# Kernel optimization log

Measured on AMD Instinct MI355X. Metric: run time of the kernel, lower is better.

Reference implementation:

```python
import jax, jax.numpy as jnp
import numpy as np


def setup_inputs() -> dict:
    key = jax.random.key(0)
    ks = jax.random.split(key, 5)
    B, H, W, C = 64, 14, 14, 2048
    x = jax.random.normal(ks[0], (B, H, W, C), dtype=jnp.float32)
    # Glorot-ish scaled 1x1 conv weights (stored as [Cin, Cout])
    W1 = jax.random.normal(ks[1], (C, 64), dtype=jnp.float32) * (1.0 / np.sqrt(C))
    W2 = jax.random.normal(ks[2], (64, 16), dtype=jnp.float32) * (1.0 / np.sqrt(64))
    W3 = jax.random.normal(ks[3], (16, 8), dtype=jnp.float32) * (1.0 / np.sqrt(16))
    W4 = jax.random.normal(ks[4], (8, 1), dtype=jnp.float32) * (1.0 / np.sqrt(8))
    return {
        "x": x,
        "W1": W1, "b1": jnp.zeros((64,), jnp.float32),
        "W2": W2, "b2": jnp.zeros((16,), jnp.float32),
        "W3": W3, "b3": jnp.zeros((8,), jnp.float32),
        "W4": W4, "b4": jnp.zeros((1,), jnp.float32),
    }


def reference(x, W1, b1, W2, b2, W3, b3, W4, b4):
    # Dropout is identity at inference time.
    # 1x1 convs == per-pixel matmuls over channel dim.
    h = jax.nn.relu(jnp.einsum('bhwc,cd->bhwd', x, W1) + b1)   # [B,H,W,64]
    h = jax.nn.relu(jnp.einsum('bhwc,cd->bhwd', h, W2) + b2)   # [B,H,W,16]
    h = jax.nn.relu(jnp.einsum('bhwc,cd->bhwd', h, W3) + b3)   # [B,H,W,8]
    a = jax.nn.sigmoid(jnp.einsum('bhwc,cd->bhwd', h, W4) + b4)  # [B,H,W,1]
    # 'upsample' frozen ones-conv == broadcast of a over 2048 channels.
    gap_features = jnp.mean(a * x, axis=(1, 2))  # [B, 2048]
    gap_mask = jnp.mean(a, axis=(1, 2))          # [B, 1] (same value for all 2048 chans)
    return gap_features / gap_mask               # [B, 2048]
```

## Files before the change

### kernel.cpp

```cpp
#include <hip/hip_runtime.h>
#include <math.h>

#define NPIX 12544
#define CIN  2048
#define NB   64
#define PPIX 196
#define BPIMG 14
#define PXB  14
#define NBLK (NB * BPIMG)

typedef short  bf16x8 __attribute__((ext_vector_type(8)));
typedef short  bf16x4 __attribute__((ext_vector_type(4)));
typedef float  f32x4  __attribute__((ext_vector_type(4)));

__device__ inline unsigned short f2bf(float f) {
    unsigned int u = __float_as_uint(f);
    u = (u + 0x7fffu + ((u >> 16) & 1u)) >> 16;
    return (unsigned short)u;
}
__device__ inline float bf2f(unsigned short u) {
    return __uint_as_float((unsigned int)u << 16);
}

__global__ __launch_bounds__(256) void conv_w1(
    const float* __restrict__ W1, unsigned short* __restrict__ W1t)
{
    const int id = blockIdx.x * 256 + threadIdx.x;
    const int n = id >> 11;
    const int k = id & 2047;
    W1t[id] = f2bf(W1[k * 64 + n]);
}

__global__ __launch_bounds__(512, 4) void fused_attn_gap(
    const float* __restrict__ x, const unsigned short* __restrict__ W1t,
    const float* __restrict__ b1,
    const float* __restrict__ W2, const float* __restrict__ b2,
    const float* __restrict__ W3, const float* __restrict__ b3,
    const float* __restrict__ W4, const float* __restrict__ b4,
    float* __restrict__ part2, float* __restrict__ asum_part)
{
    __shared__ short xs[256 * 16 * 8];
    __shared__ float h1s[16][68];
    __shared__ float h2s[16][16];
    __shared__ float h3s[16][8];
    __shared__ float a_s[16];

    const int t    = threadIdx.x;
    const int wv   = t >> 6;
    const int lane = t & 63;
    const int l15  = lane & 15;
    const int q    = lane >> 4;
    const int blk  = blockIdx.x;
    const size_t pix0 = (size_t)blk * PXB;

    const int tp = t >> 5;
    const int tc = t & 31;
    float4 xv[16];
    if (tp < PXB) {
        const float* xp = x + (pix0 + tp) * (size_t)CIN + tc * 4;
#pragma unroll
        for (int i = 0; i < 16; ++i)
            xv[i] = *(const float4*)(xp + i * 128);
    } else {
#pragma unroll
        for (int i = 0; i < 16; ++i) xv[i] = make_float4(0.f, 0.f, 0.f, 0.f);
    }
    if (t < 256)
        *(f32x4*)&h1s[t >> 4][(t & 15) * 4] = *(const f32x4*)(b1 + (t & 15) * 4);
#pragma unroll
    for (int i = 0; i < 16; ++i) {
        const int k = tc * 4 + i * 128;
        const int g = k >> 3;
        const int e = k & 7;
        bf16x4 w;
        w[0] = (short)f2bf(xv[i].x); w[1] = (short)f2bf(xv[i].y);
        w[2] = (short)f2bf(xv[i].z); w[3] = (short)f2bf(xv[i].w);
        *(bf16x4*)&xs[(g * 16 + tp) * 8 + e] = w;
    }
    __syncthreads();

    const unsigned short* wr = W1t + (size_t)l15 * CIN + wv * 256 + q * 8;
    const bf16x8* xsv = (const bf16x8*)xs;
    const int gq = wv * 32 + q;

    f32x4 acc[4] = {{0,0,0,0},{0,0,0,0},{0,0,0,0},{0,0,0,0}};
    bf16x8 wA[4], wB[4];
#pragma unroll
    for (int ct = 0; ct < 4; ++ct)
        wA[ct] = *(const bf16x8*)(wr + (size_t)ct * 16 * CIN);
#pragma unroll
    for (int i = 0; i < 8; ++i) {
        if (i < 7) {
            if ((i & 1) == 0) {
#pragma unroll
                for (int ct = 0; ct < 4; ++ct)
                    wB[ct] = *(const bf16x8*)(wr + (size_t)ct * 16 * CIN + 32 * (i + 1));
            } else {
#pragma unroll
                for (int ct = 0; ct < 4; ++ct)
                    wA[ct] = *(const bf16x8*)(wr + (size_t)ct * 16 * CIN + 32 * (i + 1));
            }
        }
        const bf16x8 av = xsv[(gq + i * 4) * 16 + l15];
        if ((i & 1) == 0) {
#pragma unroll
            for (int ct = 0; ct < 4; ++ct)
                acc[ct] = __builtin_amdgcn_mfma_f32_16x16x32_bf16(av, wA[ct], acc[ct], 0, 0, 0);
        } else {
#pragma unroll
            for (int ct = 0; ct < 4; ++ct)
                acc[ct] = __builtin_amdgcn_mfma_f32_16x16x32_bf16(av, wB[ct], acc[ct], 0, 0, 0);
        }
    }
#pragma unroll
    for (int ct = 0; ct < 4; ++ct)
#pragma unroll
        for (int r = 0; r < 4; ++r)
            atomicAdd(&h1s[q * 4 + r][ct * 16 + l15], acc[ct][r]);
    __syncthreads();

    const int p = t >> 4;
    const int j = t & 15;
    if (t < 256) {
        float s = b2[j];
#pragma unroll
        for (int k = 0; k < 64; ++k)
            s = fmaf(fmaxf(h1s[p][k], 0.f), W2[k * 16 + j], s);
        h2s[p][j] = fmaxf(s, 0.f);
    }
    __syncthreads();
    if (t < 256 && j < 8) {
        float s = b3[j];
#pragma unroll
        for (int k = 0; k < 16; ++k) s = fmaf(h2s[p][k], W3[k * 8 + j], s);
        h3s[p][j] = fmaxf(s, 0.f);
    }
    __syncthreads();
    if (t < 256 && j == 0) {
        float z = b4[0];
#pragma unroll
        for (int k = 0; k < 8; ++k) z = fmaf(h3s[p][k], W4[k], z);
        a_s[p] = (p < PXB) ? (1.f / (1.f + expf(-z))) : 0.f;
    }
    __syncthreads();

    if (t == 0) {
        float s = 0.f;
#pragma unroll
        for (int pp = 0; pp < PXB; ++pp) s += a_s[pp];
        asum_part[blk] = s;
    }

    const float ap = a_s[l15];
#pragma unroll
    for (int gi = 0; gi < 8; ++gi) {
        const int g = wv * 32 + q * 8 + gi;
        const bf16x8 v = xsv[g * 16 + l15];
        float sarr[8];
#pragma unroll
        for (int e = 0; e < 8; ++e)
            sarr[e] = ap * bf2f((unsigned short)v[e]);
#pragma unroll
        for (int m = 1; m < 16; m <<= 1)
#pragma unroll
            for (int e = 0; e < 8; ++e)
                sarr[e] += __shfl_xor(sarr[e], m, 16);
        if (l15 == 0) {
            float* dst = part2 + (size_t)blk * CIN + g * 8;
            *(float4*)dst       = make_float4(sarr[0], sarr[1], sarr[2], sarr[3]);
            *(float4*)(dst + 4) = make_float4(sarr[4], sarr[5], sarr[6], sarr[7]);
        }
    }
}

__global__ __launch_bounds__(512) void gap_final(
    const float* __restrict__ asum_part, const float* __restrict__ part2,
    float* __restrict__ out)
{
    __shared__ float red[16];
    const int b = blockIdx.x, t = threadIdx.x;
    if (t < 16) red[t] = (t < BPIMG) ? asum_part[b * BPIMG + t] : 0.f;
    __syncthreads();
    float s = 0.f;
#pragma unroll
    for (int z = 0; z < BPIMG; ++z) s += red[z];
    const float inv = 1.f / s;

    const int c0 = t * 4;
    float4 acc = {0.f, 0.f, 0.f, 0.f};
#pragma unroll
    for (int z = 0; z < BPIMG; ++z) {
        const float4 pv = *(const float4*)(part2 + (size_t)(b * BPIMG + z) * CIN + c0);
        acc.x += pv.x; acc.y += pv.y; acc.z += pv.z; acc.w += pv.w;
    }
    float4 r;
    r.x = acc.x * inv; r.y = acc.y * inv; r.z = acc.z * inv; r.w = acc.w * inv;
    *(float4*)(out + (size_t)b * CIN + c0) = r;
}

extern "C" void kernel_launch(void* const* d_in, const int* in_sizes, int n_in,
                              void* d_out, int out_size, void* d_ws, size_t ws_size,
                              hipStream_t stream)
{
    const float* x  = (const float*)d_in[0];
    const float* W1 = (const float*)d_in[1];
    const float* b1 = (const float*)d_in[2];
    const float* W2 = (const float*)d_in[3];
    const float* b2 = (const float*)d_in[4];
    const float* W3 = (const float*)d_in[5];
    const float* b3 = (const float*)d_in[6];
    const float* W4 = (const float*)d_in[7];
    const float* b4 = (const float*)d_in[8];
    float* out = (float*)d_out;

    unsigned short* W1t = (unsigned short*)d_ws;
    float* asum_part = (float*)((char*)d_ws + (512 << 10));
    float* part2     = (float*)((char*)d_ws + (1 << 20));

    conv_w1<<<512, 256, 0, stream>>>(W1, W1t);
    fused_attn_gap<<<NBLK, 512, 0, stream>>>(x, W1t, b1, W2, b2, W3, b3, W4, b4,
                                             part2, asum_part);
    gap_final<<<NB, 512, 0, stream>>>(asum_part, part2, out);
}
```

Baseline: 235.2 us.

## Load x directly to LDS via global_load_lds, halve pixels per block, prepack W1 fragments

Pixels per block drop from 14 to 7, which doubles the grid to 1792 blocks. The x tile is now copied as fp32 straight into LDS with swizzled global_load_lds, replacing the register staging and bf16 conversion. A-fragments are converted to bf16 on the fly from LDS, and W1 is pre-permuted into MFMA fragment order so each lane loads it contiguously. The weighted GAP reduction now reads exact fp32 x from LDS per channel without shuffles, which removes the bf16 rounding in that sum. In exchange, LDS per block rises to 56KB, the MFMA rows for pixels 7 to 15 duplicate work, and gap_final has twice as many partials to add.

```diff
diff --git a/kernel.cpp b/kernel.cpp
--- a/kernel.cpp
+++ b/kernel.cpp
@@ -5,12 +5,11 @@
 #define CIN  2048
 #define NB   64
 #define PPIX 196
-#define BPIMG 14
-#define PXB  14
+#define PXB  7
+#define BPIMG 28
 #define NBLK (NB * BPIMG)
 
 typedef short  bf16x8 __attribute__((ext_vector_type(8)));
-typedef short  bf16x4 __attribute__((ext_vector_type(4)));
 typedef float  f32x4  __attribute__((ext_vector_type(4)));
 
 __device__ inline unsigned short f2bf(float f) {
@@ -18,28 +17,31 @@
     u = (u + 0x7fffu + ((u >> 16) & 1u)) >> 16;
     return (unsigned short)u;
 }
-__device__ inline float bf2f(unsigned short u) {
-    return __uint_as_float((unsigned int)u << 16);
-}
 
 __global__ __launch_bounds__(256) void conv_w1(
-    const float* __restrict__ W1, unsigned short* __restrict__ W1t)
-{
-    const int id = blockIdx.x * 256 + threadIdx.x;
-    const int n = id >> 11;
-    const int k = id & 2047;
-    W1t[id] = f2bf(W1[k * 64 + n]);
-}
-
-__global__ __launch_bounds__(512, 4) void fused_attn_gap(
-    const float* __restrict__ x, const unsigned short* __restrict__ W1t,
+    const float* __restrict__ W1, unsigned short* __restrict__ Wf)
+{
+    const int o    = blockIdx.x * 256 + threadIdx.x;
+    const int e    = o & 7;
+    const int lane = (o >> 3) & 63;
+    const int ct   = (o >> 9) & 3;
+    const int i    = (o >> 11) & 7;
+    const int wv   = (o >> 14) & 7;
+    const int q = lane >> 4, l15 = lane & 15;
+    const int n = ct * 16 + l15;
+    const int k = wv * 256 + i * 32 + q * 8 + e;
+    Wf[o] = f2bf(W1[k * 64 + n]);
+}
+
+__global__ __launch_bounds__(512) void fused_attn_gap(
+    const float* __restrict__ x, const unsigned short* __restrict__ Wf,
     const float* __restrict__ b1,
     const float* __restrict__ W2, const float* __restrict__ b2,
     const float* __restrict__ W3, const float* __restrict__ b3,
     const float* __restrict__ W4, const float* __restrict__ b4,
     float* __restrict__ part2, float* __restrict__ asum_part)
 {
-    __shared__ short xs[256 * 16 * 8];
+    __shared__ float xs[PXB * CIN];
     __shared__ float h1s[16][68];
     __shared__ float h2s[16][16];
     __shared__ float h3s[16][8];
@@ -53,63 +55,55 @@
     const int blk  = blockIdx.x;
     const size_t pix0 = (size_t)blk * PXB;
 
-    const int tp = t >> 5;
-    const int tc = t & 31;
-    float4 xv[16];
-    if (tp < PXB) {
-        const float* xp = x + (pix0 + tp) * (size_t)CIN + tc * 4;
-#pragma unroll
-        for (int i = 0; i < 16; ++i)
-            xv[i] = *(const float4*)(xp + i * 128);
-    } else {
-#pragma unroll
-        for (int i = 0; i < 16; ++i) xv[i] = make_float4(0.f, 0.f, 0.f, 0.f);
+#pragma unroll
+    for (int r = 0; r < PXB; ++r) {
+        const int swb = r << 4;
+        const float* gsrc = x + (pix0 + r) * (size_t)CIN + wv * 256
+                          + (((lane * 16) ^ swb) >> 2);
+        __builtin_amdgcn_global_load_lds(gsrc, &xs[r * CIN + wv * 256], 16, 0, 0);
     }
     if (t < 256)
         *(f32x4*)&h1s[t >> 4][(t & 15) * 4] = *(const f32x4*)(b1 + (t & 15) * 4);
-#pragma unroll
-    for (int i = 0; i < 16; ++i) {
-        const int k = tc * 4 + i * 128;
-        const int g = k >> 3;
-        const int e = k & 7;
-        bf16x4 w;
-        w[0] = (short)f2bf(xv[i].x); w[1] = (short)f2bf(xv[i].y);
-        w[2] = (short)f2bf(xv[i].z); w[3] = (short)f2bf(xv[i].w);
-        *(bf16x4*)&xs[(g * 16 + tp) * 8 + e] = w;
-    }
-    __syncthreads();
-
-    const unsigned short* wr = W1t + (size_t)l15 * CIN + wv * 256 + q * 8;
-    const bf16x8* xsv = (const bf16x8*)xs;
-    const int gq = wv * 32 + q;
+    __syncthreads();
+
+    int rm = l15; if (rm >= 7) rm -= 7; if (rm >= 7) rm -= 7;
+    const int sw = rm << 4;
+    const char* xrow = (const char*)&xs[rm * CIN];
 
     f32x4 acc[4] = {{0,0,0,0},{0,0,0,0},{0,0,0,0},{0,0,0,0}};
     bf16x8 wA[4], wB[4];
 #pragma unroll
     for (int ct = 0; ct < 4; ++ct)
-        wA[ct] = *(const bf16x8*)(wr + (size_t)ct * 16 * CIN);
+        wA[ct] = *(const bf16x8*)(Wf + ((size_t)((wv * 8 + 0) * 4 + ct)) * 512 + lane * 8);
 #pragma unroll
     for (int i = 0; i < 8; ++i) {
         if (i < 7) {
             if ((i & 1) == 0) {
 #pragma unroll
                 for (int ct = 0; ct < 4; ++ct)
-                    wB[ct] = *(const bf16x8*)(wr + (size_t)ct * 16 * CIN + 32 * (i + 1));
+                    wB[ct] = *(const bf16x8*)(Wf + ((size_t)((wv * 8 + i + 1) * 4 + ct)) * 512 + lane * 8);
             } else {
 #pragma unroll
                 for (int ct = 0; ct < 4; ++ct)
-                    wA[ct] = *(const bf16x8*)(wr + (size_t)ct * 16 * CIN + 32 * (i + 1));
+                    wA[ct] = *(const bf16x8*)(Wf + ((size_t)((wv * 8 + i + 1) * 4 + ct)) * 512 + lane * 8);
             }
         }
-        const bf16x8 av = xsv[(gq + i * 4) * 16 + l15];
+        const int b0 = wv * 1024 + i * 128 + q * 32;
+        const f32x4 lo = *(const f32x4*)(xrow + ((b0)      ^ sw));
+        const f32x4 hi = *(const f32x4*)(xrow + ((b0 + 16) ^ sw));
+        bf16x8 af;
+        af[0] = (short)f2bf(lo[0]); af[1] = (short)f2bf(lo[1]);
+        af[2] = (short)f2bf(lo[2]); af[3] = (short)f2bf(lo[3]);
+        af[4] = (short)f2bf(hi[0]); af[5] = (short)f2bf(hi[1]);
+        af[6] = (short)f2bf(hi[2]); af[7] = (short)f2bf(hi[3]);
         if ((i & 1) == 0) {
 #pragma unroll
             for (int ct = 0; ct < 4; ++ct)
-                acc[ct] = __builtin_amdgcn_mfma_f32_16x16x32_bf16(av, wA[ct], acc[ct], 0, 0, 0);
+                acc[ct] = __builtin_amdgcn_mfma_f32_16x16x32_bf16(af, wA[ct], acc[ct], 0, 0, 0);
         } else {
 #pragma unroll
             for (int ct = 0; ct < 4; ++ct)
-                acc[ct] = __builtin_amdgcn_mfma_f32_16x16x32_bf16(av, wB[ct], acc[ct], 0, 0, 0);
+                acc[ct] = __builtin_amdgcn_mfma_f32_16x16x32_bf16(af, wB[ct], acc[ct], 0, 0, 0);
         }
     }
 #pragma unroll
@@ -144,32 +138,21 @@
     }
     __syncthreads();
 
+    f32x4 s = {0.f, 0.f, 0.f, 0.f};
+#pragma unroll
+    for (int pp = 0; pp < PXB; ++pp) {
+        const f32x4 v = *(const f32x4*)((const char*)xs + pp * 8192
+                                        + ((t * 16) ^ (pp << 4)));
+        const float ap = a_s[pp];
+        s[0] = fmaf(ap, v[0], s[0]); s[1] = fmaf(ap, v[1], s[1]);
+        s[2] = fmaf(ap, v[2], s[2]); s[3] = fmaf(ap, v[3], s[3]);
+    }
+    *(f32x4*)(part2 + (size_t)blk * CIN + t * 4) = s;
     if (t == 0) {
-        float s = 0.f;
-#pragma unroll
-        for (int pp = 0; pp < PXB; ++pp) s += a_s[pp];
-        asum_part[blk] = s;
-    }
-
-    const float ap = a_s[l15];
-#pragma unroll
-    for (int gi = 0; gi < 8; ++gi) {
-        const int g = wv * 32 + q * 8 + gi;
-        const bf16x8 v = xsv[g * 16 + l15];
-        float sarr[8];
-#pragma unroll
-        for (int e = 0; e < 8; ++e)
-            sarr[e] = ap * bf2f((unsigned short)v[e]);
-#pragma unroll
-        for (int m = 1; m < 16; m <<= 1)
-#pragma unroll
-            for (int e = 0; e < 8; ++e)
-                sarr[e] += __shfl_xor(sarr[e], m, 16);
-        if (l15 == 0) {
-            float* dst = part2 + (size_t)blk * CIN + g * 8;
-            *(float4*)dst       = make_float4(sarr[0], sarr[1], sarr[2], sarr[3]);
-            *(float4*)(dst + 4) = make_float4(sarr[4], sarr[5], sarr[6], sarr[7]);
-        }
+        float sa = 0.f;
+#pragma unroll
+        for (int pp = 0; pp < PXB; ++pp) sa += a_s[pp];
+        asum_part[blk] = sa;
     }
 }
 
@@ -177,25 +160,24 @@
     const float* __restrict__ asum_part, const float* __restrict__ part2,
     float* __restrict__ out)
 {
-    __shared__ float red[16];
+    __shared__ float red[BPIMG];
     const int b = blockIdx.x, t = threadIdx.x;
-    if (t < 16) red[t] = (t < BPIMG) ? asum_part[b * BPIMG + t] : 0.f;
-    __syncthreads();
-    float s = 0.f;
-#pragma unroll
-    for (int z = 0; z < BPIMG; ++z) s += red[z];
-    const float inv = 1.f / s;
+    if (t < BPIMG) red[t] = asum_part[b * BPIMG + t];
+    __syncthreads();
+    float ssum = 0.f;
+#pragma unroll
+    for (int z = 0; z < BPIMG; ++z) ssum += red[z];
+    const float inv = 1.f / ssum;
 
     const int c0 = t * 4;
-    float4 acc = {0.f, 0.f, 0.f, 0.f};
+    f32x4 acc = {0.f, 0.f, 0.f, 0.f};
 #pragma unroll
     for (int z = 0; z < BPIMG; ++z) {
-        const float4 pv = *(const float4*)(part2 + (size_t)(b * BPIMG + z) * CIN + c0);
-        acc.x += pv.x; acc.y += pv.y; acc.z += pv.z; acc.w += pv.w;
-    }
-    float4 r;
-    r.x = acc.x * inv; r.y = acc.y * inv; r.z = acc.z * inv; r.w = acc.w * inv;
-    *(float4*)(out + (size_t)b * CIN + c0) = r;
+        const f32x4 pv = *(const f32x4*)(part2 + (size_t)(b * BPIMG + z) * CIN + c0);
+        acc += pv;
+    }
+    f32x4 r = acc * inv;
+    *(f32x4*)(out + (size_t)b * CIN + c0) = r;
 }
 
 extern "C" void kernel_launch(void* const* d_in, const int* in_sizes, int n_in,
@@ -213,12 +195,12 @@
     const float* b4 = (const float*)d_in[8];
     float* out = (float*)d_out;
 
-    unsigned short* W1t = (unsigned short*)d_ws;
+    unsigned short* Wf = (unsigned short*)d_ws;
     float* asum_part = (float*)((char*)d_ws + (512 << 10));
     float* part2     = (float*)((char*)d_ws + (1 << 20));
 
-    conv_w1<<<512, 256, 0, stream>>>(W1, W1t);
-    fused_attn_gap<<<NBLK, 512, 0, stream>>>(x, W1t, b1, W2, b2, W3, b3, W4, b4,
+    conv_w1<<<512, 256, 0, stream>>>(W1, Wf);
+    fused_attn_gap<<<NBLK, 512, 0, stream>>>(x, Wf, b1, W2, b2, W3, b3, W4, b4,
                                              part2, asum_part);
     gap_final<<<NB, 512, 0, stream>>>(asum_part, part2, out);
 }
```

New measurement: 248.3 us. 5.6% more time.
